# Optimization experiments

Measured on AMD Instinct MI355X. Metric: run time of the kernel, lower is better.

## Reference

```python
import jax, jax.numpy as jnp
import numpy as np

B, N, E, D = 4, 4096, 2048, 128
MAX_L = 10


def setup_inputs() -> dict:
    key = jax.random.key(0)
    ks = jax.random.split(key, 8)
    x = jax.random.normal(ks[0], (B, N, D), dtype=jnp.float32)
    incidence = jax.random.uniform(ks[1], (B, N, E), dtype=jnp.float32)
    edge_orders = jax.random.randint(ks[2], (B, E), 0, MAX_L + 1)
    # positive normalizer to avoid division blow-up
    prefix_normalizer = jax.random.uniform(ks[3], (B, E), dtype=jnp.float32) + 0.5
    node_mask = jnp.ones((B, N), dtype=bool)
    edge_mask = jnp.ones((B, E), dtype=bool)
    n_nodes = jnp.full((B,), float(N), dtype=jnp.float32)
    # learned tables: Positional2DWeight(2, max_l+1, D, D) and PositionalWeight(max_l+1, 1, D)
    w_table = jax.random.normal(ks[4], (2, MAX_L + 1, D, D), dtype=jnp.float32) * (1.0 / np.sqrt(D))
    b_table = jax.random.normal(ks[5], (MAX_L + 1, D), dtype=jnp.float32) * 0.02
    return {"x": x, "incidence": incidence, "edge_orders": edge_orders,
            "prefix_normalizer": prefix_normalizer, "node_mask": node_mask,
            "edge_mask": edge_mask, "n_nodes": n_nodes,
            "w_table": w_table, "b_table": b_table}


def reference(x, incidence, edge_orders, prefix_normalizer, node_mask, edge_mask,
              n_nodes, w_table, b_table):
    # mask invalid nodes
    x = jnp.where(node_mask[..., None], x, 0.0)  # [B,N,D]
    # per-edge weight gather (the duplicated [B,E,D,D] tensors)
    w0 = w_table[0][edge_orders]  # [B,E,D,D]
    w1 = w_table[1][edge_orders]  # [B,E,D,D]
    w0_1 = w_table[0, 1]          # [D,D]
    w1_1 = w_table[1, 1]          # [D,D]
    # global mean pooling over nodes
    x0 = jnp.sum(x, axis=1, keepdims=True) / n_nodes[:, None, None]  # [B,1,D]
    # incidence-based V2E aggregation
    x1_e = jnp.einsum('bne,bnd->bed', incidence, x) / prefix_normalizer[..., None]
    x1_e = jnp.where(edge_mask[..., None], x1_e, 0.0)  # [B,E,D]
    # node branch: shared order-1 weights
    x_v = jnp.einsum('bnd,do->bno', x0, w0_1) + jnp.einsum('bnd,do->bno', x, w1_1)
    # edge branch: per-edge-order weights
    x_e = jnp.einsum('bd,bedo->beo', x0[:, 0], w0) + jnp.einsum('bed,bedo->beo', x1_e, w1)
    x_v = jnp.where(node_mask[..., None], x_v, 0.0)
    x_e = jnp.where(edge_mask[..., None], x_e, 0.0)
    # BiasE
    bias_e = b_table[edge_orders]            # [B,E,D]
    bias_1 = b_table[1][None, None, :]       # [1,1,D]
    x_v = jnp.where(node_mask[..., None], x_v + bias_1, 0.0)
    x_e = jnp.where(edge_mask[..., None], x_e + bias_e, 0.0)
    return x_v, x_e
```

## Files before the change

### kernel.cpp

```cpp
#include <hip/hip_runtime.h>

#define Bb 4
#define Nn 4096
#define Ee 2048
#define Dd 128
#define NL 11
#define NTMAX 560
#define ZS 4
#define NB_EIN (Bb * (Ee / 32) * ZS)
#define NB_XV (Bb * (Nn / 64))
#define NB_TRX 2048
#define NB_PACK 8192

typedef unsigned short u16;
typedef unsigned int u32;
typedef __attribute__((ext_vector_type(8))) short short8;
typedef __attribute__((ext_vector_type(4))) float floatx4;

__device__ __forceinline__ u32 pk2(float lo, float hi) {
    u32 r;
    asm("v_cvt_pk_bf16_f32 %0, %1, %2" : "=v"(r) : "v"(lo), "v"(hi));
    return r;
}
union S8U { u32 u[4]; short8 s; };

__global__ __launch_bounds__(256) void k_prep(const float* __restrict__ x,
                                              const float* __restrict__ inc,
                                              const float* __restrict__ wt,
                                              const int* __restrict__ ord,
                                              u32* __restrict__ xt,
                                              u32* __restrict__ inct,
                                              float* __restrict__ part,
                                              u32* __restrict__ wt1T,
                                              int* __restrict__ cnt,
                                              int* __restrict__ offs,
                                              int* __restrict__ idx,
                                              int* __restrict__ tilemap) {
    __shared__ float tP[32][129];
    __shared__ float tT[32][33];
    __shared__ int ib[3 * Bb * NL];
    int blk = blockIdx.x, t = threadIdx.x;
    if (blk < NB_TRX) {
        int b = blk & 3, n0b = (blk >> 2) & 127, d0b = blk >> 9;
        int n0 = n0b * 32, d0 = d0b * 32;
        int r = t >> 5, c = t & 31;
#pragma unroll
        for (int i = 0; i < 4; i++)
            tT[r + 8 * i][c] = x[((size_t)b * Nn + n0 + r + 8 * i) * Dd + d0 + c];
        __syncthreads();
#pragma unroll
        for (int i = 0; i < 2; i++) {
            int idx2 = t + 256 * i;
            int dl = idx2 >> 4, cp = idx2 & 15;
            u32 v = pk2(tT[2 * cp][dl], tT[2 * cp + 1][dl]);
            xt[(size_t)(b * Dd + d0 + dl) * (Nn / 2) + (n0 >> 1) + cp] = v;
        }
        if (t < 32) {
            float s = 0.f;
#pragma unroll
            for (int rr = 0; rr < 32; rr++) s += tT[rr][t];
            part[((size_t)(b * 4 + d0b) * 128 + n0b) * 32 + t] = s;
        }
    } else if (blk < NB_TRX + NB_PACK) {
        int rr = blk - NB_TRX;
        int b = rr & 3, nb = (rr >> 2) & 127, ebg = rr >> 9;
        int n0 = nb * 32, e0 = ebg * 128;
        int r = t >> 3, c4 = t & 7;
        const float* src = inc + ((size_t)b * Nn + n0 + r) * Ee + e0 + c4 * 16;
#pragma unroll
        for (int k = 0; k < 4; k++)
            *(float4*)&tP[r][c4 * 16 + k * 4] = *(const float4*)(src + k * 4);
        __syncthreads();
        int ol = t >> 1, half = t & 1;
        u32* op = inct + (size_t)(b * Ee + e0 + ol) * (Nn / 2) + nb * 16 + half * 8;
#pragma unroll
        for (int np = 0; np < 8; np++) {
            int pair = half * 8 + np;
            op[np] = pk2(tP[2 * pair][ol], tP[2 * pair + 1][ol]);
        }
    } else if (blk < NB_TRX + NB_PACK + 176) {
        int rr = blk - (NB_TRX + NB_PACK);
        int l = rr >> 4, sub = rr & 15;
        int d0 = (sub >> 2) * 32, o0 = (sub & 3) * 32;
        const float* w1 = wt + (size_t)(NL + l) * Dd * Dd;
        int r = t >> 5, c = t & 31;
#pragma unroll
        for (int i = 0; i < 4; i++)
            tT[r + 8 * i][c] = w1[(size_t)(d0 + r + 8 * i) * Dd + o0 + c];
        __syncthreads();
#pragma unroll
        for (int i = 0; i < 2; i++) {
            int idx2 = t + 256 * i;
            int ol = idx2 >> 4, dp = idx2 & 15;
            u32 v = pk2(tT[2 * dp][ol], tT[2 * dp + 1][ol]);
            wt1T[(size_t)(l * Dd + o0 + ol) * (Dd / 2) + (d0 >> 1) + dp] = v;
        }
    } else {
        int* scnt = ib;
        int* soff = ib + Bb * NL;
        int* scur = ib + 2 * Bb * NL;
        if (t < Bb * NL) { scnt[t] = 0; scur[t] = 0; }
        __syncthreads();
        for (int g = t; g < Bb * Ee; g += 256)
            atomicAdd(&scnt[(g >> 11) * NL + ord[g]], 1);
        __syncthreads();
        if (t == 0) {
            int off = 0, pos = 0;
            for (int i = 0; i < Bb * NL; i++) {
                soff[i] = off;
                offs[i] = off;
                cnt[i] = scnt[i];
                int al = (scnt[i] + 15) & ~15;
                off += al;
                for (int j = 0; j < (al >> 4); j++) tilemap[pos++] = (i << 16) | j;
            }
            for (; pos < NTMAX; pos++) tilemap[pos] = -1;
        }
        for (int i = t; i < 8960; i += 256) idx[i] = 0;
        __syncthreads();
        for (int g = t; g < Bb * Ee; g += 256) {
            int bk = (g >> 11) * NL + ord[g];
            int pos = soff[bk] + atomicAdd(&scur[bk], 1);
            idx[pos] = g & 2047;
        }
    }
}

__global__ __launch_bounds__(128) void k_xe0(const float* __restrict__ part,
                                             const float* __restrict__ wt,
                                             const float* __restrict__ bt,
                                             float* __restrict__ xe0b) {
    int b = blockIdx.x, l = blockIdx.y, o = threadIdx.x;
    __shared__ float ssum[Dd];
    const float* pp = part + ((size_t)(b * 4 + (o >> 5)) * 128) * 32 + (o & 31);
    float s = 0.f;
    for (int nb = 0; nb < 128; nb++) s += pp[nb * 32];
    ssum[o] = s;
    __syncthreads();
    const float* w0 = wt + (size_t)l * Dd * Dd + o;
    float acc = 0.f;
    for (int d = 0; d < Dd; ++d) acc += ssum[d] * w0[(size_t)d * Dd];
    xe0b[(b * NL + l) * Dd + o] = acc * (1.0f / Nn) + bt[l * Dd + o];
}

__global__ __launch_bounds__(256) void k_main(const u32* __restrict__ inct,
                                              const u32* __restrict__ xt,
                                              const float* __restrict__ x,
                                              const u32* __restrict__ wt1T,
                                              const float* __restrict__ xe0b,
                                              float* __restrict__ x1p,
                                              float* __restrict__ outv) {
    int blk = blockIdx.x, t = threadIdx.x;
    int w = t >> 6, lane = t & 63, lm = lane & 15, quad = lane >> 4;
    if (blk < NB_EIN) {
        int b = blk & 3, et0 = ((blk >> 2) & 63) * 32, s = blk >> 8;
        int nbase = s * (Nn / ZS);
        const u32* ap0 = inct + (size_t)(b * Ee + et0 + lm) * (Nn / 2) + (nbase >> 1);
        const u32* ap1 = ap0 + (size_t)16 * (Nn / 2);
        const u32* bp0 = xt + (size_t)(b * Dd + w * 32 + lm) * (Nn / 2) + (nbase >> 1);
        const u32* bp1 = bp0 + (size_t)16 * (Nn / 2);
        floatx4 a00 = {0.f,0.f,0.f,0.f}, a01 = {0.f,0.f,0.f,0.f};
        floatx4 a10 = {0.f,0.f,0.f,0.f}, a11 = {0.f,0.f,0.f,0.f};
        for (int ci = 0; ci < 4; ci++) {
            int ko = ci * 128;
#pragma unroll
            for (int ks = 0; ks < 8; ks++) {
                int o = ko + ks * 16 + quad * 4;
                short8 A0 = *(const short8*)(ap0 + o);
                short8 A1 = *(const short8*)(ap1 + o);
                short8 B0 = *(const short8*)(bp0 + o);
                short8 B1 = *(const short8*)(bp1 + o);
                a00 = __builtin_amdgcn_mfma_f32_16x16x32_bf16(A0, B0, a00, 0, 0, 0);
                a01 = __builtin_amdgcn_mfma_f32_16x16x32_bf16(A0, B1, a01, 0, 0, 0);
                a10 = __builtin_amdgcn_mfma_f32_16x16x32_bf16(A1, B0, a10, 0, 0, 0);
                a11 = __builtin_amdgcn_mfma_f32_16x16x32_bf16(A1, B1, a11, 0, 0, 0);
            }
        }
        int db = w * 32 + lm;
        float* base = x1p + ((size_t)(s * Bb + b) * Ee) * Dd;
#pragma unroll
        for (int r = 0; r < 4; r++) {
            float* q0 = base + (size_t)(et0 + quad * 4 + r) * Dd;
            q0[db] = a00[r];
            q0[db + 16] = a01[r];
            float* q1 = base + (size_t)(et0 + 16 + quad * 4 + r) * Dd;
            q1[db] = a10[r];
            q1[db + 16] = a11[r];
        }
    } else {
        int rr = blk - NB_EIN;
        int b = rr & 3, n0 = (rr >> 2) * 64;
        const float* xrow = x + ((size_t)b * Nn + n0 + w * 16 + lm) * Dd;
        const u32* wrow = wt1T + (size_t)1 * Dd * (Dd / 2);
        floatx4 acc[8];
#pragma unroll
        for (int ot = 0; ot < 8; ot++) acc[ot] = (floatx4){0.f, 0.f, 0.f, 0.f};
#pragma unroll
        for (int ks = 0; ks < 4; ks++) {
            float4 va = *(const float4*)(xrow + ks * 32 + quad * 8);
            float4 vb = *(const float4*)(xrow + ks * 32 + quad * 8 + 4);
            S8U A;
            A.u[0] = pk2(va.x, va.y); A.u[1] = pk2(va.z, va.w);
            A.u[2] = pk2(vb.x, vb.y); A.u[3] = pk2(vb.z, vb.w);
#pragma unroll
            for (int ot = 0; ot < 8; ot++) {
                short8 Bf = *(const short8*)(wrow + (size_t)(ot * 16 + lm) * (Dd / 2) +
                                             ks * 16 + quad * 4);
                acc[ot] = __builtin_amdgcn_mfma_f32_16x16x32_bf16(A.s, Bf, acc[ot], 0, 0, 0);
            }
        }
#pragma unroll
        for (int ot = 0; ot < 8; ot++) {
            float basev = xe0b[(b * NL + 1) * Dd + ot * 16 + lm];
#pragma unroll
            for (int r = 0; r < 4; r++)
                outv[((size_t)b * Nn + n0 + w * 16 + quad * 4 + r) * Dd + ot * 16 + lm] =
                    acc[ot][r] + basev;
        }
    }
}

__global__ __launch_bounds__(256) void k_epi(const float* __restrict__ x1p,
                                             const float* __restrict__ pref,
                                             const u32* __restrict__ wt1T,
                                             const float* __restrict__ xe0b,
                                             const int* __restrict__ cnt,
                                             const int* __restrict__ offs,
                                             const int* __restrict__ idx,
                                             const int* __restrict__ tilemap,
                                             float* __restrict__ oute) {
    int t = threadIdx.x, w = t >> 6, lane = t & 63, lm = lane & 15, quad = lane >> 4;
    int ent = tilemap[blockIdx.x * 4 + w];
    if (ent < 0) return;
    int bk = ent >> 16, j = ent & 0xffff;
    int bb = bk / NL, l = bk % NL;
    int off = offs[bk], cntv = cnt[bk];
    int eA = idx[off + j * 16 + lm];
    float rp = 1.0f / pref[bb * Ee + eA];
    const float* p0 = x1p + ((size_t)bb * Ee + eA) * Dd;
    const u32* wrow = wt1T + (size_t)l * Dd * (Dd / 2);
    floatx4 acc[8];
#pragma unroll
    for (int ot = 0; ot < 8; ot++) acc[ot] = (floatx4){0.f, 0.f, 0.f, 0.f};
#pragma unroll
    for (int ks = 0; ks < 4; ks++) {
        int d0 = ks * 32 + quad * 8;
        float4 u0 = *(const float4*)(p0 + d0);
        float4 u1 = *(const float4*)(p0 + d0 + 4);
#pragma unroll
        for (int s = 1; s < ZS; s++) {
            const float* ps = p0 + (size_t)s * Bb * Ee * Dd;
            float4 v0 = *(const float4*)(ps + d0);
            float4 v1 = *(const float4*)(ps + d0 + 4);
            u0.x += v0.x; u0.y += v0.y; u0.z += v0.z; u0.w += v0.w;
            u1.x += v1.x; u1.y += v1.y; u1.z += v1.z; u1.w += v1.w;
        }
        S8U A;
        A.u[0] = pk2(u0.x * rp, u0.y * rp);
        A.u[1] = pk2(u0.z * rp, u0.w * rp);
        A.u[2] = pk2(u1.x * rp, u1.y * rp);
        A.u[3] = pk2(u1.z * rp, u1.w * rp);
#pragma unroll
        for (int ot = 0; ot < 8; ot++) {
            short8 Bf = *(const short8*)(wrow + (size_t)(ot * 16 + lm) * (Dd / 2) +
                                         ks * 16 + quad * 4);
            acc[ot] = __builtin_amdgcn_mfma_f32_16x16x32_bf16(A.s, Bf, acc[ot], 0, 0, 0);
        }
    }
    int4 rid = *(const int4*)&idx[off + j * 16 + quad * 4];
    int rowbase = j * 16 + quad * 4;
#pragma unroll
    for (int ot = 0; ot < 8; ot++) {
        float basev = xe0b[(bb * NL + l) * Dd + ot * 16 + lm];
#pragma unroll
        for (int r = 0; r < 4; r++) {
            if (rowbase + r < cntv) {
                int e = ((const int*)&rid)[r];
                oute[((size_t)bb * Ee + e) * Dd + ot * 16 + lm] = acc[ot][r] + basev;
            }
        }
    }
}

extern "C" void kernel_launch(void* const* d_in, const int* in_sizes, int n_in,
                              void* d_out, int out_size, void* d_ws,
                              size_t ws_size, hipStream_t stream) {
    const float* x    = (const float*)d_in[0];
    const float* inc  = (const float*)d_in[1];
    const int*   ord  = (const int*)d_in[2];
    const float* pref = (const float*)d_in[3];
    const float* wt   = (const float*)d_in[7];
    const float* bt   = (const float*)d_in[8];

    float* outv = (float*)d_out;
    float* oute = outv + (size_t)Bb * Nn * Dd;

    float* ws      = (float*)d_ws;
    float* xe0b    = ws + 512;
    int*   cnt     = (int*)(ws + 6144);
    int*   offs    = (int*)(ws + 6192);
    int*   tilemap = (int*)(ws + 6288);
    float* part    = ws + 8192;
    u32*   xt      = (u32*)(ws + 8192 + 65536);
    u32*   wt1T    = (u32*)(ws + 8192 + 65536 + 1048576);
    int*   idx     = (int*)(ws + 8192 + 65536 + 1048576 + 90112);
    float* x1p     = ws + 8192 + 65536 + 1048576 + 90112 + 8960;
    u32*   inct    = (u32*)(x1p + (size_t)ZS * Bb * Ee * Dd);

    k_prep<<<NB_TRX + NB_PACK + 176 + 1, 256, 0, stream>>>(
        x, inc, wt, ord, xt, inct, part, wt1T, cnt, offs, idx, tilemap);
    k_xe0<<<dim3(Bb, NL), 128, 0, stream>>>(part, wt, bt, xe0b);
    k_main<<<NB_EIN + NB_XV, 256, 0, stream>>>(inct, xt, x, wt1T, xe0b, x1p, outv);
    k_epi<<<NTMAX / 4, 256, 0, stream>>>(x1p, pref, wt1T, xe0b, cnt, offs, idx,
                                         tilemap, oute);
}
```

Before: 352.1 us.

## Store bf16 incidence and x in node-blocked layout for contiguous MFMA operand loads

Switches the packed bf16 incidence and transposed x buffers from a row-major [row][N/2] layout to a node-blocked [nblock][row][16] layout. Each MFMA operand fetch then reads a contiguous 64-byte chunk per 16 rows, and the incidence pack step writes 64 bytes per thread with vector stores. The pack kernel now handles 256 edges per block, halving its block count and doubling its LDS tile. k_main gets a launch-bounds occupancy hint and a reordered block-index mapping. The cost is a larger LDS footprint in k_prep and different cache locality across blocks.

```diff
diff --git a/kernel.cpp b/kernel.cpp
--- a/kernel.cpp
+++ b/kernel.cpp
@@ -7,10 +7,12 @@
 #define NL 11
 #define NTMAX 560
 #define ZS 4
+#define NBLK (Nn / 32)
 #define NB_EIN (Bb * (Ee / 32) * ZS)
 #define NB_XV (Bb * (Nn / 64))
 #define NB_TRX 2048
-#define NB_PACK 8192
+#define NB_TRI 4096
+#define NB_TRW 176
 
 typedef unsigned short u16;
 typedef unsigned int u32;
@@ -28,7 +30,7 @@
                                               const float* __restrict__ inc,
                                               const float* __restrict__ wt,
                                               const int* __restrict__ ord,
-                                              u32* __restrict__ xt,
+                                              u32* __restrict__ xtb,
                                               u32* __restrict__ inct,
                                               float* __restrict__ part,
                                               u32* __restrict__ wt1T,
@@ -36,7 +38,7 @@
                                               int* __restrict__ offs,
                                               int* __restrict__ idx,
                                               int* __restrict__ tilemap) {
-    __shared__ float tP[32][129];
+    __shared__ float tP[32][257];
     __shared__ float tT[32][33];
     __shared__ int ib[3 * Bb * NL];
     int blk = blockIdx.x, t = threadIdx.x;
@@ -53,7 +55,7 @@
             int idx2 = t + 256 * i;
             int dl = idx2 >> 4, cp = idx2 & 15;
             u32 v = pk2(tT[2 * cp][dl], tT[2 * cp + 1][dl]);
-            xt[(size_t)(b * Dd + d0 + dl) * (Nn / 2) + (n0 >> 1) + cp] = v;
+            xtb[(size_t)((b * NBLK + n0b) * Dd + d0 + dl) * 16 + cp] = v;
         }
         if (t < 32) {
             float s = 0.f;
@@ -61,25 +63,27 @@
             for (int rr = 0; rr < 32; rr++) s += tT[rr][t];
             part[((size_t)(b * 4 + d0b) * 128 + n0b) * 32 + t] = s;
         }
-    } else if (blk < NB_TRX + NB_PACK) {
+    } else if (blk < NB_TRX + NB_TRI) {
         int rr = blk - NB_TRX;
-        int b = rr & 3, nb = (rr >> 2) & 127, ebg = rr >> 9;
-        int n0 = nb * 32, e0 = ebg * 128;
-        int r = t >> 3, c4 = t & 7;
-        const float* src = inc + ((size_t)b * Nn + n0 + r) * Ee + e0 + c4 * 16;
-#pragma unroll
-        for (int k = 0; k < 4; k++)
-            *(float4*)&tP[r][c4 * 16 + k * 4] = *(const float4*)(src + k * 4);
-        __syncthreads();
-        int ol = t >> 1, half = t & 1;
-        u32* op = inct + (size_t)(b * Ee + e0 + ol) * (Nn / 2) + nb * 16 + half * 8;
-#pragma unroll
-        for (int np = 0; np < 8; np++) {
-            int pair = half * 8 + np;
-            op[np] = pk2(tP[2 * pair][ol], tP[2 * pair + 1][ol]);
-        }
-    } else if (blk < NB_TRX + NB_PACK + 176) {
-        int rr = blk - (NB_TRX + NB_PACK);
+        int b = rr & 3, nb = (rr >> 2) & 127, eg = rr >> 9;
+        int n0 = nb * 32, e0 = eg * 256;
+        const float* src = inc + ((size_t)b * Nn + n0) * Ee + e0;
+#pragma unroll
+        for (int k = 0; k < 8; k++) {
+            int f4 = t + 256 * k;
+            int r = f4 >> 6, e4 = f4 & 63;
+            *(float4*)&tP[r][e4 * 4] = *(const float4*)(src + (size_t)r * Ee + e4 * 4);
+        }
+        __syncthreads();
+        u32* op = inct + (size_t)((b * NBLK + nb) * Ee + e0 + t) * 16;
+        u32 ov[16];
+#pragma unroll
+        for (int p = 0; p < 16; p++) ov[p] = pk2(tP[2 * p][t], tP[2 * p + 1][t]);
+#pragma unroll
+        for (int p = 0; p < 4; p++)
+            *(uint4*)(op + 4 * p) = *(uint4*)(ov + 4 * p);
+    } else if (blk < NB_TRX + NB_TRI + NB_TRW) {
+        int rr = blk - (NB_TRX + NB_TRI);
         int l = rr >> 4, sub = rr & 15;
         int d0 = (sub >> 2) * 32, o0 = (sub & 3) * 32;
         const float* w1 = wt + (size_t)(NL + l) * Dd * Dd;
@@ -143,38 +147,34 @@
     xe0b[(b * NL + l) * Dd + o] = acc * (1.0f / Nn) + bt[l * Dd + o];
 }
 
-__global__ __launch_bounds__(256) void k_main(const u32* __restrict__ inct,
-                                              const u32* __restrict__ xt,
-                                              const float* __restrict__ x,
-                                              const u32* __restrict__ wt1T,
-                                              const float* __restrict__ xe0b,
-                                              float* __restrict__ x1p,
-                                              float* __restrict__ outv) {
+__global__ __launch_bounds__(256, 4) void k_main(const u32* __restrict__ inct,
+                                                 const u32* __restrict__ xtb,
+                                                 const float* __restrict__ x,
+                                                 const u32* __restrict__ wt1T,
+                                                 const float* __restrict__ xe0b,
+                                                 float* __restrict__ x1p,
+                                                 float* __restrict__ outv) {
     int blk = blockIdx.x, t = threadIdx.x;
     int w = t >> 6, lane = t & 63, lm = lane & 15, quad = lane >> 4;
     if (blk < NB_EIN) {
-        int b = blk & 3, et0 = ((blk >> 2) & 63) * 32, s = blk >> 8;
-        int nbase = s * (Nn / ZS);
-        const u32* ap0 = inct + (size_t)(b * Ee + et0 + lm) * (Nn / 2) + (nbase >> 1);
-        const u32* ap1 = ap0 + (size_t)16 * (Nn / 2);
-        const u32* bp0 = xt + (size_t)(b * Dd + w * 32 + lm) * (Nn / 2) + (nbase >> 1);
-        const u32* bp1 = bp0 + (size_t)16 * (Nn / 2);
+        int et0 = (blk & 63) * 32, b = (blk >> 6) & 3, s = blk >> 8;
+        int nb0 = s * (NBLK / ZS);
+        const u32* ap = inct + (size_t)((b * NBLK + nb0) * Ee + et0 + lm) * 16 + quad * 4;
+        const u32* bp = xtb + (size_t)((b * NBLK + nb0) * Dd + w * 32 + lm) * 16 + quad * 4;
         floatx4 a00 = {0.f,0.f,0.f,0.f}, a01 = {0.f,0.f,0.f,0.f};
         floatx4 a10 = {0.f,0.f,0.f,0.f}, a11 = {0.f,0.f,0.f,0.f};
-        for (int ci = 0; ci < 4; ci++) {
-            int ko = ci * 128;
-#pragma unroll
-            for (int ks = 0; ks < 8; ks++) {
-                int o = ko + ks * 16 + quad * 4;
-                short8 A0 = *(const short8*)(ap0 + o);
-                short8 A1 = *(const short8*)(ap1 + o);
-                short8 B0 = *(const short8*)(bp0 + o);
-                short8 B1 = *(const short8*)(bp1 + o);
-                a00 = __builtin_amdgcn_mfma_f32_16x16x32_bf16(A0, B0, a00, 0, 0, 0);
-                a01 = __builtin_amdgcn_mfma_f32_16x16x32_bf16(A0, B1, a01, 0, 0, 0);
-                a10 = __builtin_amdgcn_mfma_f32_16x16x32_bf16(A1, B0, a10, 0, 0, 0);
-                a11 = __builtin_amdgcn_mfma_f32_16x16x32_bf16(A1, B1, a11, 0, 0, 0);
-            }
+#pragma unroll 4
+        for (int ni = 0; ni < NBLK / ZS; ni++) {
+            const u32* a0 = ap + (size_t)ni * Ee * 16;
+            const u32* b0 = bp + (size_t)ni * Dd * 16;
+            short8 A0 = *(const short8*)(a0);
+            short8 A1 = *(const short8*)(a0 + 16 * 16);
+            short8 B0 = *(const short8*)(b0);
+            short8 B1 = *(const short8*)(b0 + 16 * 16);
+            a00 = __builtin_amdgcn_mfma_f32_16x16x32_bf16(A0, B0, a00, 0, 0, 0);
+            a01 = __builtin_amdgcn_mfma_f32_16x16x32_bf16(A0, B1, a01, 0, 0, 0);
+            a10 = __builtin_amdgcn_mfma_f32_16x16x32_bf16(A1, B0, a10, 0, 0, 0);
+            a11 = __builtin_amdgcn_mfma_f32_16x16x32_bf16(A1, B1, a11, 0, 0, 0);
         }
         int db = w * 32 + lm;
         float* base = x1p + ((size_t)(s * Bb + b) * Ee) * Dd;
@@ -301,16 +301,16 @@
     int*   offs    = (int*)(ws + 6192);
     int*   tilemap = (int*)(ws + 6288);
     float* part    = ws + 8192;
-    u32*   xt      = (u32*)(ws + 8192 + 65536);
+    u32*   xtb     = (u32*)(ws + 8192 + 65536);
     u32*   wt1T    = (u32*)(ws + 8192 + 65536 + 1048576);
     int*   idx     = (int*)(ws + 8192 + 65536 + 1048576 + 90112);
     float* x1p     = ws + 8192 + 65536 + 1048576 + 90112 + 8960;
     u32*   inct    = (u32*)(x1p + (size_t)ZS * Bb * Ee * Dd);
 
-    k_prep<<<NB_TRX + NB_PACK + 176 + 1, 256, 0, stream>>>(
-        x, inc, wt, ord, xt, inct, part, wt1T, cnt, offs, idx, tilemap);
+    k_prep<<<NB_TRX + NB_TRI + NB_TRW + 1, 256, 0, stream>>>(
+        x, inc, wt, ord, xtb, inct, part, wt1T, cnt, offs, idx, tilemap);
     k_xe0<<<dim3(Bb, NL), 128, 0, stream>>>(part, wt, bt, xe0b);
-    k_main<<<NB_EIN + NB_XV, 256, 0, stream>>>(inct, xt, x, wt1T, xe0b, x1p, outv);
+    k_main<<<NB_EIN + NB_XV, 256, 0, stream>>>(inct, xtb, x, wt1T, xe0b, x1p, outv);
     k_epi<<<NTMAX / 4, 256, 0, stream>>>(x1p, pref, wt1T, xe0b, cnt, offs, idx,
                                          tilemap, oute);
 }
```

After: 318.5 us. 9.5% less time.
